# Kernel optimization log

Measured on AMD Instinct MI355X. Metric: run time of the kernel, lower is better.

Reference implementation:

```python
import jax, jax.numpy as jnp
import numpy as np

B, S, T = 32, 64, 64
V_IN, V_OUT, E, H, L = 32000, 32000, 256, 512, 2


def _cell(x, h, c, Wih, Whh, bih, bhh):
    # PyTorch LSTM gate order: i, f, g, o
    z = x @ Wih.T + h @ Whh.T + bih + bhh
    i, f, g, o = jnp.split(z, 4, axis=-1)
    c2 = jax.nn.sigmoid(f) * c + jax.nn.sigmoid(i) * jnp.tanh(g)
    h2 = jax.nn.sigmoid(o) * jnp.tanh(c2)
    return h2, c2


def setup_inputs() -> dict:
    key = jax.random.key(0)
    ks = iter(jax.random.split(key, 32))
    k = 1.0 / np.sqrt(H)
    u = lambda kk, shape: jax.random.uniform(kk, shape, jnp.float32, -k, k)
    inp = {}
    inp['inputs'] = jax.random.randint(next(ks), (B, S), 0, V_IN)
    inp['targets'] = jax.random.randint(next(ks), (B, T), 0, V_OUT)
    inp['max_target_len'] = T
    lens = jax.random.randint(next(ks), (B,), 1, S + 1)
    inp['inputs_lenghts'] = jnp.sort(lens)[::-1]  # pack_padded needs descending
    inp['enc_emb'] = jax.random.normal(next(ks), (V_IN, E), jnp.float32)
    inp['dec_emb'] = jax.random.normal(next(ks), (V_OUT, E), jnp.float32)
    for pre, in0 in (('enc', E), ('dec', E)):
        for l in range(L):
            d_in = in0 if l == 0 else H
            inp[f'{pre}_Wih{l}'] = u(next(ks), (4 * H, d_in))
            inp[f'{pre}_Whh{l}'] = u(next(ks), (4 * H, H))
            inp[f'{pre}_bih{l}'] = u(next(ks), (4 * H,))
            inp[f'{pre}_bhh{l}'] = u(next(ks), (4 * H,))
    inp['fc_W'] = u(next(ks), (V_OUT, H))
    inp['fc_b'] = u(next(ks), (V_OUT,))
    return inp


def reference(inputs, targets, max_target_len, inputs_lenghts,
              enc_emb, dec_emb,
              enc_Wih0, enc_Whh0, enc_bih0, enc_bhh0,
              enc_Wih1, enc_Whh1, enc_bih1, enc_bhh1,
              dec_Wih0, dec_Whh0, dec_bih0, dec_bhh0,
              dec_Wih1, dec_Whh1, dec_bih1, dec_bhh1,
              fc_W, fc_b):
    Bsz, Slen = inputs.shape
    emb = enc_emb[inputs]                                   # [B,S,E]
    mask = jnp.arange(Slen)[None, :] < inputs_lenghts[:, None]  # [B,S]

    def enc_step(carry, xs):
        (h0, c0), (h1, c1) = carry
        x, m = xs                                           # [B,E], [B]
        m = m[:, None]
        nh0, nc0 = _cell(x, h0, c0, enc_Wih0, enc_Whh0, enc_bih0, enc_bhh0)
        h0 = jnp.where(m, nh0, h0); c0 = jnp.where(m, nc0, c0)
        nh1, nc1 = _cell(h0, h1, c1, enc_Wih1, enc_Whh1, enc_bih1, enc_bhh1)
        h1 = jnp.where(m, nh1, h1); c1 = jnp.where(m, nc1, c1)
        return ((h0, c0), (h1, c1)), None

    z = jnp.zeros((Bsz, H), emb.dtype)
    carry0 = ((z, z), (z, z))
    ((eh0, _), (eh1, _)), _ = jax.lax.scan(
        enc_step, carry0, (emb.transpose(1, 0, 2), mask.T))

    # decoder: greedy argmax feedback (eval-mode branch), c init to zeros
    tok0 = jnp.ones((Bsz,), dtype=inputs.dtype)

    def dec_step(carry, _):
        h0, c0, h1, c1, tok = carry
        x = dec_emb[tok]                                    # [B,E]
        h0, c0 = _cell(x, h0, c0, dec_Wih0, dec_Whh0, dec_bih0, dec_bhh0)
        h1, c1 = _cell(h0, h1, c1, dec_Wih1, dec_Whh1, dec_bih1, dec_bhh1)
        logits = h1 @ fc_W.T + fc_b                         # [B,V]
        tok = jnp.argmax(logits, axis=-1).astype(tok.dtype)
        return (h0, c0, h1, c1, tok), logits

    init = (eh0, jnp.zeros_like(eh0), eh1, jnp.zeros_like(eh1), tok0)
    _, logits = jax.lax.scan(dec_step, init, None, length=max_target_len)
    return logits.transpose(1, 0, 2)                        # [B,T,V]
```

## Files before the change

### kernel.cpp

```cpp
#include <hip/hip_runtime.h>
#include <cstdint>
#include <cstddef>
#include <cfloat>


#define NWG   256
#define NTHR  512
#define BSZ   32
#define SLEN  64
#define TLEN  64
#define EDIM  256
#define HDIM  512
#define VOUT  32000
#define FCWGS 250
#define FCR   128
#define FSTR  16

#define XS0 20
#define HSL 36
#define RS0 (16 * XS0 + 16 * HSL)
#define RS1 (16 * HSL + 16 * HSL)
#define HB  576
#define HGEN 16384
#define NHG_FRESH 258
#define NHG_FB    8
#define NCG_FRESH 64
#define NCG_FB    2

struct SMem {
    float w0[8 * RS0];
    float w1[8 * RS1];
    float hst[32 * HB];
    float zsh0[8 * 32];
    float zsh1[8 * 32];
    float cmv[32 * 32];
    int   cmi[32 * 32];
    float bsum0[8], bsum1[8];
    float fcb_s[FCR];
    int   tok[BSZ];
    int   llen[BSZ];
};

__device__ __forceinline__ void astore(float* p, float v) {
    __hip_atomic_store(p, v, __ATOMIC_RELAXED, __HIP_MEMORY_SCOPE_AGENT);
}
__device__ __forceinline__ void astorei(int* p, int v) {
    __hip_atomic_store(p, v, __ATOMIC_RELAXED, __HIP_MEMORY_SCOPE_AGENT);
}
__device__ __forceinline__ float2 aload2(const float* p) {
    unsigned long long u = __hip_atomic_load((const unsigned long long*)p,
                              __ATOMIC_RELAXED, __HIP_MEMORY_SCOPE_AGENT);
    union { unsigned long long u; float2 f; } c; c.u = u; return c.f;
}

__device__ __forceinline__ int fbmap(int g) {
    if (g < 65)  return (g & 1);
    if (g < 130) return 2 + ((g - 65) & 1);
    if (g < 194) return 4 + ((g - 130) & 1);
    return 6 + ((g - 194) & 1);
}
__device__ __forceinline__ float* genp(float* hb, int g, int fresh) {
    return hb + (size_t)(fresh ? g : fbmap(g)) * HGEN;
}

__device__ __forceinline__ void gridbar(unsigned* flags, unsigned* sense,
                                        unsigned& epoch)
{
    asm volatile("s_waitcnt vmcnt(0)" ::: "memory");
    __syncthreads();
    epoch++;
    const int tid = threadIdx.x;
    if (tid == 0)
        __hip_atomic_store(&flags[(size_t)blockIdx.x * FSTR], epoch,
                           __ATOMIC_RELAXED, __HIP_MEMORY_SCOPE_AGENT);
    if (blockIdx.x == 0) {
        if (tid < 64) {
#pragma unroll
            for (int k = 0; k < 4; k++) {
                const size_t idx = (size_t)(tid * 4 + k) * FSTR;
                while (__hip_atomic_load(&flags[idx], __ATOMIC_RELAXED,
                                         __HIP_MEMORY_SCOPE_AGENT) < epoch)
                    __builtin_amdgcn_s_sleep(2);
            }
        }
        __syncthreads();
        if (tid == 0)
            __hip_atomic_store(sense, epoch, __ATOMIC_RELAXED,
                               __HIP_MEMORY_SCOPE_AGENT);
    }
    if (tid == 0) {
        while (__hip_atomic_load(sense, __ATOMIC_RELAXED,
                                 __HIP_MEMORY_SCOPE_AGENT) < epoch)
            __builtin_amdgcn_s_sleep(4);
    }
    __syncthreads();
}

__device__ __forceinline__ void stage_h(float* hst, const float* __restrict__ hg,
                                        int cached)
{
    const int t = threadIdx.x;
    if (cached) {
#pragma unroll
        for (int i = 0; i < 8; i++) {
            int f = i * 2048 + t * 4;
            float4 v = *(const float4*)(hg + f);
            int b = f >> 9, j = f & 511;
            *(float4*)(&hst[b * HB + (j >> 5) * 36 + (j & 31)]) = v;
        }
    } else {
#pragma unroll
        for (int i = 0; i < 16; i++) {
            int f = i * 1024 + t * 2;
            float2 v = aload2(hg + f);
            int b = f >> 9, j = f & 511;
            *(float2*)(&hst[b * HB + (j >> 5) * 36 + (j & 31)]) = v;
        }
    }
}
__device__ __forceinline__ void read_slice32(const float* hst, int b, int kq,
                                             float* dst)
{
#pragma unroll
    for (int i = 0; i < 8; i++) {
        float4 v = *(const float4*)(hst + b * HB + kq * 36 + i * 4);
        dst[i * 4 + 0] = v.x; dst[i * 4 + 1] = v.y;
        dst[i * 4 + 2] = v.z; dst[i * 4 + 3] = v.w;
    }
}

template<int KIN>
__device__ __forceinline__ void stage_w(float* dst,
        const float* __restrict__ Wih, const float* __restrict__ Whh,
        const float* __restrict__ bih, const float* __restrict__ bhh,
        float* bsum, int j0)
{
    constexpr int XC = KIN / 16;
    constexpr int XS = (KIN == 256) ? XS0 : HSL;
    constexpr int RS = (KIN == 256) ? RS0 : RS1;
    const int tid = threadIdx.x;
    constexpr int nf4x = KIN / 4;
    for (int tt = tid; tt < 8 * nf4x; tt += NTHR) {
        int r = tt / nf4x, k = (tt % nf4x) * 4;
        int row = (r >> 1) * HDIM + j0 + (r & 1);
        float4 v = *(const float4*)(Wih + (size_t)row * KIN + k);
        *(float4*)(dst + r * RS + (k / XC) * XS + (k % XC)) = v;
    }
    for (int tt = tid; tt < 8 * 128; tt += NTHR) {
        int r = tt >> 7, k = (tt & 127) * 4;
        int row = (r >> 1) * HDIM + j0 + (r & 1);
        float4 v = *(const float4*)(Whh + (size_t)row * HDIM + k);
        *(float4*)(dst + r * RS + 16 * XS + (k >> 5) * HSL + (k & 31)) = v;
    }
    if (tid < 8) {
        int row = (tid >> 1) * HDIM + j0 + (tid & 1);
        bsum[tid] = bih[row] + bhh[row];
    }
}

template<int KIN>
__device__ __forceinline__ void cell_compute(SMem& sm, const float* __restrict__ w,
        const float* bsum, const float* xv, const float* hv,
        float* __restrict__ hout, float& creg, bool domask, int s, int j0,
        float* zsh)
{
    constexpr int XC = KIN / 16;
    constexpr int XS = (KIN == 256) ? XS0 : HSL;
    constexpr int RS = (KIN == 256) ? RS0 : RS1;
    const int tid = threadIdx.x;
    const int wave = tid >> 6, lane = tid & 63, kq = lane & 15, bl = lane >> 4;
    const int b = wave * 4 + bl;

#pragma unroll
    for (int r = 0; r < 8; r++) {
        float acc = 0.f;
        const float* wx = w + r * RS + kq * XS;
#pragma unroll
        for (int i = 0; i < XC / 4; i++) {
            float4 t4 = *(const float4*)(wx + i * 4);
            acc += t4.x * xv[i*4] + t4.y * xv[i*4+1] + t4.z * xv[i*4+2] + t4.w * xv[i*4+3];
        }
        const float* wh = w + r * RS + 16 * XS + kq * HSL;
#pragma unroll
        for (int i = 0; i < 8; i++) {
            float4 t4 = *(const float4*)(wh + i * 4);
            acc += t4.x * hv[i*4] + t4.y * hv[i*4+1] + t4.z * hv[i*4+2] + t4.w * hv[i*4+3];
        }
        acc += __shfl_xor(acc, 1);
        acc += __shfl_xor(acc, 2);
        acc += __shfl_xor(acc, 4);
        acc += __shfl_xor(acc, 8);
        if (kq == 0) zsh[r * 32 + b] = acc + bsum[r];
    }
    __syncthreads();
    if (tid < 64) {
        int jl = tid >> 5, bb = tid & 31;
        float zi = zsh[(0 + jl) * 32 + bb];
        float zf = zsh[(2 + jl) * 32 + bb];
        float zg = zsh[(4 + jl) * 32 + bb];
        float zo = zsh[(6 + jl) * 32 + bb];
        float iv = 1.f / (1.f + expf(-zi));
        float fv = 1.f / (1.f + expf(-zf));
        float gv = tanhf(zg);
        float ov = 1.f / (1.f + expf(-zo));
        float cold = creg;
        float c2 = fv * cold + iv * gv;
        float h2 = ov * tanhf(c2);
        int j = j0 + jl;
        if (domask) {
            bool m = s < sm.llen[bb];
            if (!m) {
                h2 = sm.hst[bb * HB + (j >> 5) * 36 + (j & 31)];
                c2 = cold;
            }
        }
        astore(hout + (size_t)bb * HDIM + j, h2);
        creg = c2;
    }
}

__device__ __forceinline__ void fc_run(SMem& sm, const float4 (&wfc)[4][8],
        const float* __restrict__ h1g, float* __restrict__ out, int t, int g,
        float* __restrict__ cand_val, int* __restrict__ cand_idx, int cached)
{
    const int tid = threadIdx.x;
    const int kh = tid & 15, rg = tid >> 4;
    const int v0 = g * FCR;

    stage_h(sm.hst, h1g, cached);
    __syncthreads();

    float bias[4];
#pragma unroll
    for (int r = 0; r < 4; r++) bias[r] = sm.fcb_s[rg * 4 + r];

    for (int b = 0; b < 32; b++) {
        float hv[32];
        read_slice32(sm.hst, b, kh, hv);
        float a0 = 0.f, a1 = 0.f, a2 = 0.f, a3 = 0.f;
#pragma unroll
        for (int i = 0; i < 8; i++) {
            float4 w0 = wfc[0][i], w1 = wfc[1][i], w2 = wfc[2][i], w3 = wfc[3][i];
            float h0 = hv[i*4], h1 = hv[i*4+1], h2 = hv[i*4+2], h3 = hv[i*4+3];
            a0 += w0.x * h0 + w0.y * h1 + w0.z * h2 + w0.w * h3;
            a1 += w1.x * h0 + w1.y * h1 + w1.z * h2 + w1.w * h3;
            a2 += w2.x * h0 + w2.y * h1 + w2.z * h2 + w2.w * h3;
            a3 += w3.x * h0 + w3.y * h1 + w3.z * h2 + w3.w * h3;
        }
#pragma unroll
        for (int m = 1; m < 16; m <<= 1) {
            a0 += __shfl_xor(a0, m);
            a1 += __shfl_xor(a1, m);
            a2 += __shfl_xor(a2, m);
            a3 += __shfl_xor(a3, m);
        }
        if (kh == 0) {
            float z0 = a0 + bias[0], z1 = a1 + bias[1];
            float z2 = a2 + bias[2], z3 = a3 + bias[3];
            *(float4*)(out + ((size_t)b * TLEN + t) * VOUT + v0 + rg * 4)
                = make_float4(z0, z1, z2, z3);
            float lm = z0; int li = 0;
            if (z1 > lm) { lm = z1; li = 1; }
            if (z2 > lm) { lm = z2; li = 2; }
            if (z3 > lm) { lm = z3; li = 3; }
            sm.cmv[rg * 32 + b] = lm;
            sm.cmi[rg * 32 + b] = v0 + rg * 4 + li;
        }
    }
    __syncthreads();
    if (tid < 32) {
        float bv = sm.cmv[tid]; int bi = sm.cmi[tid];
#pragma unroll
        for (int r2 = 1; r2 < 32; r2++) {
            float v = sm.cmv[r2 * 32 + tid]; int ix = sm.cmi[r2 * 32 + tid];
            if (v > bv || (v == bv && ix < bi)) { bv = v; bi = ix; }
        }
        astore(&cand_val[(size_t)tid * NWG + g], bv);
        astorei(&cand_idx[(size_t)tid * NWG + g], bi);
    }
}

__global__ __launch_bounds__(NTHR, 2)
void seq2seq_persist(
    const int* __restrict__ inputs, const int* __restrict__ lens,
    const float* __restrict__ enc_emb, const float* __restrict__ dec_emb,
    const float* __restrict__ eW0ih, const float* __restrict__ eW0hh,
    const float* __restrict__ eB0ih, const float* __restrict__ eB0hh,
    const float* __restrict__ eW1ih, const float* __restrict__ eW1hh,
    const float* __restrict__ eB1ih, const float* __restrict__ eB1hh,
    const float* __restrict__ dW0ih, const float* __restrict__ dW0hh,
    const float* __restrict__ dB0ih, const float* __restrict__ dB0hh,
    const float* __restrict__ dW1ih, const float* __restrict__ dW1hh,
    const float* __restrict__ dB1ih, const float* __restrict__ dB1hh,
    const float* __restrict__ fcW, const float* __restrict__ fcb,
    float* __restrict__ out,
    float* hb, float* cb, unsigned* flags, unsigned* sense, int fresh)
{
    __shared__ SMem sm;
    const int g = blockIdx.x;
    const int tid = threadIdx.x;
    const int j0 = g * 2;
    unsigned epoch = 0;

    __builtin_amdgcn_fence(__ATOMIC_ACQUIRE, "agent");

    const int wave = tid >> 6, lane = tid & 63, kq16 = lane & 15, bl = lane >> 4;
    const int b = wave * 4 + bl;

    if (tid < 64) {
        astore(&genp(hb, 0, fresh)[g * 64 + tid], 0.f);
        astore(&genp(hb, 65, fresh)[g * 64 + tid], 0.f);
    }
    stage_w<EDIM>(sm.w0, eW0ih, eW0hh, eB0ih, eB0hh, sm.bsum0, j0);
    stage_w<HDIM>(sm.w1, eW1ih, eW1hh, eB1ih, eB1hh, sm.bsum1, j0);
    if (tid < BSZ) sm.llen[tid] = lens[tid];
    float c0r = 0.f, c1r = 0.f;
    gridbar(flags, sense, epoch);

    for (int s = 0; s <= SLEN; ++s) {
        stage_h(sm.hst, genp(hb, s, fresh), fresh);
        __syncthreads();
        float xv0[16], hv0[32], xv1[32];
        if (s < SLEN) {
            int tokv = inputs[b * SLEN + s];
            const float* x0 = enc_emb + (size_t)tokv * EDIM;
#pragma unroll
            for (int i = 0; i < 4; i++) {
                float4 v = *(const float4*)(x0 + kq16 * 16 + i * 4);
                xv0[i*4] = v.x; xv0[i*4+1] = v.y; xv0[i*4+2] = v.z; xv0[i*4+3] = v.w;
            }
            read_slice32(sm.hst, b, kq16, hv0);
        }
        if (s >= 1) read_slice32(sm.hst, b, kq16, xv1);
        if (s < SLEN)
            cell_compute<EDIM>(sm, sm.w0, sm.bsum0, xv0, hv0,
                               genp(hb, s + 1, fresh), c0r, true, s, j0, sm.zsh0);
        __syncthreads();
        if (s >= 1) {
            stage_h(sm.hst, genp(hb, 65 + s - 1, fresh), fresh);
            __syncthreads();
            float hv1[32];
            read_slice32(sm.hst, b, kq16, hv1);
            cell_compute<HDIM>(sm, sm.w1, sm.bsum1, xv1, hv1,
                               genp(hb, 65 + s, fresh), c1r, true, s - 1, j0, sm.zsh1);
        }
        gridbar(flags, sense, epoch);
    }

    stage_w<EDIM>(sm.w0, dW0ih, dW0hh, dB0ih, dB0hh, sm.bsum0, j0);
    stage_w<HDIM>(sm.w1, dW1ih, dW1hh, dB1ih, dB1hh, sm.bsum1, j0);
    float4 wfc[4][8];
    {
        const int kh = tid & 15, rg = tid >> 4;
        if (g < FCWGS) {
            const float* wp = fcW + ((size_t)g * FCR + rg * 4) * HDIM + kh * 32;
#pragma unroll
            for (int r = 0; r < 4; r++)
#pragma unroll
                for (int i = 0; i < 8; i++)
                    wfc[r][i] = *(const float4*)(wp + (size_t)r * HDIM + i * 4);
            for (int i = tid; i < FCR; i += NTHR) sm.fcb_s[i] = fcb[g * FCR + i];
        }
    }
    c0r = 0.f; c1r = 0.f;
    __syncthreads();

    for (int t = 0; t < TLEN; ++t) {
        if (t == 0) {
            if (tid < BSZ) sm.tok[tid] = 1;
        } else {
            const float* cvp = cb + (size_t)(fresh ? (t - 1) : ((t - 1) & 1)) * HGEN;
            const float* cip = cvp + 8192;
            if (fresh) {
#pragma unroll
                for (int i = 0; i < 4; i++) {
                    int f = i * 2048 + tid * 4;
                    *(float4*)(sm.hst + f) = *(const float4*)(cvp + f);
                    *(float4*)(sm.hst + 8192 + f) = *(const float4*)(cip + f);
                }
            } else {
#pragma unroll
                for (int i = 0; i < 8; i++) {
                    int f = i * 1024 + tid * 2;
                    *(float2*)(sm.hst + f) = aload2(cvp + f);
                    *(float2*)(sm.hst + 8192 + f) = aload2(cip + f);
                }
            }
            __syncthreads();
            if (tid < 256) {
                int bq = tid >> 3, q = tid & 7;
                float bv = -FLT_MAX; int bi = 0x7fffffff;
                for (int gg = q; gg < FCWGS; gg += 8) {
                    float v = sm.hst[bq * 256 + gg];
                    int ix = ((const int*)sm.hst)[8192 + bq * 256 + gg];
                    if (v > bv || (v == bv && ix < bi)) { bv = v; bi = ix; }
                }
#pragma unroll
                for (int m = 1; m < 8; m <<= 1) {
                    float ov = __shfl_xor(bv, m); int oi = __shfl_xor(bi, m);
                    if (ov > bv || (ov == bv && oi < bi)) { bv = ov; bi = oi; }
                }
                if (q == 0) sm.tok[bq] = bi;
            }
        }
        __syncthreads();
        const int g0i = (t == 0) ? 64 : 129 + t;
        const int g0o = 129 + t + 1;
        const int g1i = (t == 0) ? 129 : 193 + t;
        const int g1o = 193 + t + 1;
        stage_h(sm.hst, genp(hb, g0i, fresh), fresh);
        __syncthreads();
        {
            const float* x0 = dec_emb + (size_t)sm.tok[b] * EDIM;
            float xv0[16], hv0[32];
#pragma unroll
            for (int i = 0; i < 4; i++) {
                float4 v = *(const float4*)(x0 + kq16 * 16 + i * 4);
                xv0[i*4] = v.x; xv0[i*4+1] = v.y; xv0[i*4+2] = v.z; xv0[i*4+3] = v.w;
            }
            read_slice32(sm.hst, b, kq16, hv0);
            cell_compute<EDIM>(sm, sm.w0, sm.bsum0, xv0, hv0,
                               genp(hb, g0o, fresh), c0r, false, 0, j0, sm.zsh0);
        }
        gridbar(flags, sense, epoch);
        stage_h(sm.hst, genp(hb, g0o, fresh), fresh);
        __syncthreads();
        float xv1[32];
        read_slice32(sm.hst, b, kq16, xv1);
        __syncthreads();
        stage_h(sm.hst, genp(hb, g1i, fresh), fresh);
        __syncthreads();
        {
            float hv1[32];
            read_slice32(sm.hst, b, kq16, hv1);
            cell_compute<HDIM>(sm, sm.w1, sm.bsum1, xv1, hv1,
                               genp(hb, g1o, fresh), c1r, false, 0, j0, sm.zsh1);
        }
        gridbar(flags, sense, epoch);
        if (g < FCWGS) {
            float* cvt = cb + (size_t)(fresh ? t : (t & 1)) * HGEN;
            fc_run(sm, wfc, genp(hb, g1o, fresh), out, t, g,
                   cvt, (int*)(cvt + 8192), fresh);
        }
        if (t < TLEN - 1)
            gridbar(flags, sense, epoch);
    }
}

__global__ void initk(unsigned* flags)
{
    int i = blockIdx.x * 256 + threadIdx.x;
    if (i < NWG * FSTR + 16) flags[i] = 0u;
}

extern "C" void kernel_launch(void* const* d_in, const int* in_sizes, int n_in,
                              void* d_out, int out_size, void* d_ws, size_t ws_size,
                              hipStream_t stream)
{
    const int*   inputs  = (const int*)d_in[0];
    const int*   lens    = (const int*)d_in[3];
    const float* enc_emb = (const float*)d_in[4];
    const float* dec_emb = (const float*)d_in[5];
    const float* W[16];
    for (int i = 0; i < 16; i++) W[i] = (const float*)d_in[6 + i];
    const float* fcW = (const float*)d_in[22];
    const float* fcb = (const float*)d_in[23];
    float* out = (float*)d_out;

    float* ws = (float*)d_ws;
    unsigned* flags = (unsigned*)ws;
    float* hb = ws + 8192;
    size_t needB = (size_t)(8192 + (NHG_FRESH + NCG_FRESH) * HGEN) * 4;
    int fresh = (ws_size >= needB) ? 1 : 0;
    float* cb = hb + (size_t)(fresh ? NHG_FRESH : NHG_FB) * HGEN;

    initk<<<17, 256, 0, stream>>>(flags);
    seq2seq_persist<<<NWG, NTHR, 0, stream>>>(
        inputs, lens, enc_emb, dec_emb,
        W[0], W[1], W[2], W[3], W[4], W[5], W[6], W[7],
        W[8], W[9], W[10], W[11], W[12], W[13], W[14], W[15],
        fcW, fcb, out,
        hb, cb, flags, flags + NWG * FSTR, fresh);
}
```

Baseline: 4.732 ms.

## Use decentralized all-poll grid barrier and prefetch layer-1 hidden state into registers

The grid barrier drops the centralized master block and sense flag. Every block now polls all 256 flags directly with 256 threads and a shorter sleep, removing one serial hop per barrier at the cost of more polling traffic on L2. Separately, the layer-1 hidden-state generation is loaded into registers at the start of each step and committed to shared memory later, so its global load latency overlaps the layer-0 cell work. This raises register pressure through 16 extra float2 values per thread.

```diff
diff --git a/kernel.cpp b/kernel.cpp
--- a/kernel.cpp
+++ b/kernel.cpp
@@ -63,8 +63,7 @@
     return hb + (size_t)(fresh ? g : fbmap(g)) * HGEN;
 }
 
-__device__ __forceinline__ void gridbar(unsigned* flags, unsigned* sense,
-                                        unsigned& epoch)
+__device__ __forceinline__ void gridbar(unsigned* flags, unsigned& epoch)
 {
     asm volatile("s_waitcnt vmcnt(0)" ::: "memory");
     __syncthreads();
@@ -73,25 +72,10 @@
     if (tid == 0)
         __hip_atomic_store(&flags[(size_t)blockIdx.x * FSTR], epoch,
                            __ATOMIC_RELAXED, __HIP_MEMORY_SCOPE_AGENT);
-    if (blockIdx.x == 0) {
-        if (tid < 64) {
-#pragma unroll
-            for (int k = 0; k < 4; k++) {
-                const size_t idx = (size_t)(tid * 4 + k) * FSTR;
-                while (__hip_atomic_load(&flags[idx], __ATOMIC_RELAXED,
-                                         __HIP_MEMORY_SCOPE_AGENT) < epoch)
-                    __builtin_amdgcn_s_sleep(2);
-            }
-        }
-        __syncthreads();
-        if (tid == 0)
-            __hip_atomic_store(sense, epoch, __ATOMIC_RELAXED,
-                               __HIP_MEMORY_SCOPE_AGENT);
-    }
-    if (tid == 0) {
-        while (__hip_atomic_load(sense, __ATOMIC_RELAXED,
+    if (tid < NWG) {
+        while (__hip_atomic_load(&flags[(size_t)tid * FSTR], __ATOMIC_RELAXED,
                                  __HIP_MEMORY_SCOPE_AGENT) < epoch)
-            __builtin_amdgcn_s_sleep(4);
+            __builtin_amdgcn_s_sleep(1);
     }
     __syncthreads();
 }
@@ -116,6 +100,30 @@
             int b = f >> 9, j = f & 511;
             *(float2*)(&hst[b * HB + (j >> 5) * 36 + (j & 31)]) = v;
         }
+    }
+}
+__device__ __forceinline__ void prefetch_h(float2* pre, const float* __restrict__ hg,
+                                           int cached)
+{
+    const int t = threadIdx.x;
+    if (cached) {
+#pragma unroll
+        for (int i = 0; i < 16; i++)
+            pre[i] = *(const float2*)(hg + i * 1024 + t * 2);
+    } else {
+#pragma unroll
+        for (int i = 0; i < 16; i++)
+            pre[i] = aload2(hg + i * 1024 + t * 2);
+    }
+}
+__device__ __forceinline__ void commit_h(float* hst, const float2* pre)
+{
+    const int t = threadIdx.x;
+#pragma unroll
+    for (int i = 0; i < 16; i++) {
+        int f = i * 1024 + t * 2;
+        int b = f >> 9, j = f & 511;
+        *(float2*)(&hst[b * HB + (j >> 5) * 36 + (j & 31)]) = pre[i];
     }
 }
 __device__ __forceinline__ void read_slice32(const float* hst, int b, int kq,
@@ -294,7 +302,7 @@
     const float* __restrict__ dB1ih, const float* __restrict__ dB1hh,
     const float* __restrict__ fcW, const float* __restrict__ fcb,
     float* __restrict__ out,
-    float* hb, float* cb, unsigned* flags, unsigned* sense, int fresh)
+    float* hb, float* cb, unsigned* flags, int fresh)
 {
     __shared__ SMem sm;
     const int g = blockIdx.x;
@@ -315,9 +323,12 @@
     stage_w<HDIM>(sm.w1, eW1ih, eW1hh, eB1ih, eB1hh, sm.bsum1, j0);
     if (tid < BSZ) sm.llen[tid] = lens[tid];
     float c0r = 0.f, c1r = 0.f;
-    gridbar(flags, sense, epoch);
+    gridbar(flags, epoch);
 
     for (int s = 0; s <= SLEN; ++s) {
+        float2 pre[16];
+        if (s >= 1)
+            prefetch_h(pre, genp(hb, 64 + s, fresh), fresh);
         stage_h(sm.hst, genp(hb, s, fresh), fresh);
         __syncthreads();
         float xv0[16], hv0[32], xv1[32];
@@ -337,14 +348,14 @@
                                genp(hb, s + 1, fresh), c0r, true, s, j0, sm.zsh0);
         __syncthreads();
         if (s >= 1) {
-            stage_h(sm.hst, genp(hb, 65 + s - 1, fresh), fresh);
+            commit_h(sm.hst, pre);
             __syncthreads();
             float hv1[32];
             read_slice32(sm.hst, b, kq16, hv1);
             cell_compute<HDIM>(sm, sm.w1, sm.bsum1, xv1, hv1,
                                genp(hb, 65 + s, fresh), c1r, true, s - 1, j0, sm.zsh1);
         }
-        gridbar(flags, sense, epoch);
+        gridbar(flags, epoch);
     }
 
     stage_w<EDIM>(sm.w0, dW0ih, dW0hh, dB0ih, dB0hh, sm.bsum0, j0);
@@ -366,6 +377,12 @@
     __syncthreads();
 
     for (int t = 0; t < TLEN; ++t) {
+        const int g0i = (t == 0) ? 64 : 129 + t;
+        const int g0o = 129 + t + 1;
+        const int g1i = (t == 0) ? 129 : 193 + t;
+        const int g1o = 193 + t + 1;
+        float2 pre[16];
+        prefetch_h(pre, genp(hb, g1i, fresh), fresh);
         if (t == 0) {
             if (tid < BSZ) sm.tok[tid] = 1;
         } else {
@@ -404,10 +421,6 @@
             }
         }
         __syncthreads();
-        const int g0i = (t == 0) ? 64 : 129 + t;
-        const int g0o = 129 + t + 1;
-        const int g1i = (t == 0) ? 129 : 193 + t;
-        const int g1o = 193 + t + 1;
         stage_h(sm.hst, genp(hb, g0i, fresh), fresh);
         __syncthreads();
         {
@@ -422,13 +435,13 @@
             cell_compute<EDIM>(sm, sm.w0, sm.bsum0, xv0, hv0,
                                genp(hb, g0o, fresh), c0r, false, 0, j0, sm.zsh0);
         }
-        gridbar(flags, sense, epoch);
+        gridbar(flags, epoch);
         stage_h(sm.hst, genp(hb, g0o, fresh), fresh);
         __syncthreads();
         float xv1[32];
         read_slice32(sm.hst, b, kq16, xv1);
         __syncthreads();
-        stage_h(sm.hst, genp(hb, g1i, fresh), fresh);
+        commit_h(sm.hst, pre);
         __syncthreads();
         {
             float hv1[32];
@@ -436,14 +449,14 @@
             cell_compute<HDIM>(sm, sm.w1, sm.bsum1, xv1, hv1,
                                genp(hb, g1o, fresh), c1r, false, 0, j0, sm.zsh1);
         }
-        gridbar(flags, sense, epoch);
+        gridbar(flags, epoch);
         if (g < FCWGS) {
             float* cvt = cb + (size_t)(fresh ? t : (t & 1)) * HGEN;
             fc_run(sm, wfc, genp(hb, g1o, fresh), out, t, g,
                    cvt, (int*)(cvt + 8192), fresh);
         }
         if (t < TLEN - 1)
-            gridbar(flags, sense, epoch);
+            gridbar(flags, epoch);
     }
 }
 
@@ -480,5 +493,5 @@
         W[0], W[1], W[2], W[3], W[4], W[5], W[6], W[7],
         W[8], W[9], W[10], W[11], W[12], W[13], W[14], W[15],
         fcW, fcb, out,
-        hb, cb, flags, flags + NWG * FSTR, fresh);
-}
+        hb, cb, flags, fresh);
+}
```

New measurement: 5.102 ms. +7.8%, slower.
